# Kernel optimization log

Measured on AMD Instinct MI355X. Metric: run time of the kernel, lower is better.

## Reference

```python
import jax, jax.numpy as jnp
import numpy as np

B, N, C, K, KS, OC = 8, 4096, 64, 20, 16, 64


def setup_inputs() -> dict:
    key = jax.random.key(0)
    ks = jax.random.split(key, 6)
    return {
        'x': jax.random.normal(ks[0], (B, 3, N), jnp.float32),
        'feature': jax.random.normal(ks[1], (B, C, N), jnp.float32),
        'kernals': jax.random.normal(ks[2], (3, KS), jnp.float32),
        'mlp_w': jax.random.normal(ks[3], (C, 7), jnp.float32) * 0.1,
        'mlp_b': jnp.zeros((C,), jnp.float32),
        'conv_w': jax.random.normal(ks[4], (OC, 2 * C * KS), jnp.float32) * 0.02,
        'conv_b': jnp.zeros((OC,), jnp.float32),
        'bn_gamma': jnp.ones((OC,), jnp.float32),
        'bn_beta': jnp.zeros((OC,), jnp.float32),
    }


def reference(x, feature, kernals, mlp_w, mlp_b, conv_w, conv_b, bn_gamma, bn_beta):
    b, _, n = x.shape
    c = feature.shape[1]
    ksz = kernals.shape[1]
    k = K
    # ---- knn on coords ----
    xt = jnp.swapaxes(x, 1, 2)                      # [B,N,3]
    inner = -2.0 * jnp.einsum('bnc,bmc->bnm', xt, xt)
    xx = jnp.sum(xt * xt, axis=-1)                  # [B,N]
    pd = -xx[:, :, None] - inner - xx[:, None, :]   # negative squared dist
    idx = jax.lax.top_k(pd, k)[1]                   # [B,N,K] nearest (incl. self)
    gather = jax.vmap(lambda pts, i: pts[i])        # per-batch gather
    # ---- geometric features ----
    x_sp = gather(xt, idx)                          # [B,N,K,3]
    x_rel = x_sp - x_sp[:, :, 0:1, :]               # [B,N,K,3]
    x_dis = jnp.linalg.norm(x_rel, axis=-1, keepdims=True)
    center = jnp.broadcast_to(x_sp[:, :, 0:1, :], x_sp.shape)
    x_feats7 = jnp.concatenate([center, x_rel, x_dis], axis=-1)  # [B,N,K,7]
    # Conv1d(7,C,1) == pointwise linear over the 7 channels
    x_feats = jnp.einsum('bnkc,oc->bnok', x_feats7, mlp_w) + mlp_b[None, None, :, None]  # [B,N,C,K]
    # ---- neighbor feature gather ----
    ft = jnp.swapaxes(feature, 1, 2)                # [B,N,C]
    sp_f = gather(ft, idx)                          # [B,N,K,C]
    spirals = jnp.concatenate([jnp.swapaxes(sp_f, 2, 3), x_feats], axis=2)  # [B,N,2C,K]
    # ---- adjacency weights ----
    one_pad = jnp.zeros((k, ksz), jnp.float32).at[0, 0].set(1.0)
    aw = jnp.einsum('bnkc,cs->bnks', x_rel, kernals) + one_pad   # [B,N,K,KS]
    aw = jnp.where(aw > 0, aw, 0.0)
    aw = aw / (jnp.sum(aw, axis=2, keepdims=True) + 1e-6)
    aw = aw * aw
    aw = aw / (jnp.sum(aw, axis=2, keepdims=True) + 1e-6)
    aw = jnp.where(aw > 0.1, aw, 0.0)
    # ---- weighted aggregation + linear ----
    agg = jnp.einsum('bnck,bnks->bncs', spirals, aw)             # [B,N,2C,KS]
    agg = agg.reshape(b, n, 2 * c * ksz)
    out = agg @ conv_w.T + conv_b                                # [B,N,OC]
    out = jnp.swapaxes(out, 1, 2)                                # [B,OC,N]
    # ---- BatchNorm1d (training-mode batch statistics, eps=1e-5) ----
    mean = jnp.mean(out, axis=(0, 2), keepdims=True)
    var = jnp.var(out, axis=(0, 2), keepdims=True)
    out = (out - mean) / jnp.sqrt(var + 1e-5)
    out = out * bn_gamma[None, :, None] + bn_beta[None, :, None]
    return out
```

## Files before the change

kernel.cpp:

```cpp
#include <hip/hip_runtime.h>
#include <cfloat>
#include <math.h>

#define NB 8
#define NPT 4096
#define NC 64
#define KNN 20
#define KSZ 16
#define BPTS 8

typedef __attribute__((ext_vector_type(8))) short short8;
typedef __attribute__((ext_vector_type(4))) float f32x4;

__device__ __forceinline__ unsigned short f2bf(float f) {
  unsigned u = __float_as_uint(f);
  unsigned r = (u + 0x7fffu + ((u >> 16) & 1u)) >> 16;
  return (unsigned short)r;
}
__device__ __forceinline__ float bf2f(unsigned short h) {
  return __uint_as_float(((unsigned)h) << 16);
}

__global__ void k_pack_cw(const float* __restrict__ cw, unsigned short* __restrict__ bp) {
  int t = blockIdx.x * 256 + threadIdx.x;
  int j = t & 7, lane = (t >> 3) & 63, nt = (t >> 9) & 3, ks = t >> 11;
  int k = ks * 32 + ((lane >> 4) << 3) + j;
  int o = nt * 16 + (lane & 15);
  bp[t] = f2bf(cw[o * 2048 + k]);
}

__global__ void k_pack_cw2(const float* __restrict__ cw, const float* __restrict__ mlp_w,
                           const float* __restrict__ mlp_b, unsigned short* __restrict__ bp2) {
  int t = blockIdx.x * 256 + threadIdx.x;
  int jj = t & 7, lane = (t >> 3) & 63, nt = (t >> 9) & 3, ks2 = t >> 11;
  int k = ks2 * 32 + ((lane >> 4) << 3) + jj;
  int s = k >> 3, j = k & 7;
  int o = nt * 16 + (lane & 15);
  float acc = 0.0f;
  for (int c = 0; c < 64; ++c) {
    float coef = (j < 7) ? mlp_w[c * 7 + j] : mlp_b[c];
    acc = fmaf(cw[o * 2048 + 1024 + c * 16 + s], coef, acc);
  }
  bp2[t] = f2bf(acc);
}

__global__ void k_transpose_ft(const float* __restrict__ f, unsigned short* __restrict__ ft) {
  __shared__ float tile[64][65];
  int b = blockIdx.x >> 6;
  int n0 = (blockIdx.x & 63) * 64;
  int lane = threadIdx.x & 63;
  int rr = threadIdx.x >> 6;
#pragma unroll
  for (int c0 = 0; c0 < 64; c0 += 4) {
    int c = c0 + rr;
    tile[c][lane] = f[(b * 64 + c) * 4096 + n0 + lane];
  }
  __syncthreads();
#pragma unroll
  for (int m0 = 0; m0 < 64; m0 += 4) {
    int nn = m0 + rr;
    ft[(b * 4096 + n0 + nn) * 64 + lane] = f2bf(tile[lane][nn]);
  }
}

__device__ __noinline__ void knn_full(const float4* __restrict__ pts, int n, int lane,
                                      int g, int* __restrict__ idxOut) {
  const int M = 24;
  float4 qp = pts[n];
  float qx = qp.x, qy = qp.y, qz = qp.z;
  float v[M];
  int id[M];
#pragma unroll
  for (int r = 0; r < M; ++r) { v[r] = FLT_MAX; id[r] = 0x7fffffff; }
  for (int i = 0; i < 64; ++i) {
    int j = (i << 6) | lane;
    float4 p = pts[j];
    float dx = p.x - qx, dy = p.y - qy, dz = p.z - qz;
    float d2 = fmaf(dx, dx, fmaf(dy, dy, dz * dz));
    bool c[M];
#pragma unroll
    for (int r = 0; r < M; ++r) c[r] = d2 < v[r];
#pragma unroll
    for (int r = M - 1; r >= 1; --r) {
      v[r] = c[r - 1] ? v[r - 1] : (c[r] ? d2 : v[r]);
      id[r] = c[r - 1] ? id[r - 1] : (c[r] ? j : id[r]);
    }
    v[0] = c[0] ? d2 : v[0];
    id[0] = c[0] ? j : id[0];
  }
  unsigned long long key = ((unsigned long long)__float_as_uint(v[0]) << 32) | (unsigned)id[0];
  unsigned long long ext = ~0ull;
  for (int r = 0; r < 24; ++r) {
    unsigned long long k = key;
#pragma unroll
    for (int s = 1; s < 64; s <<= 1) {
      unsigned long long o = __shfl_xor(k, s, 64);
      k = (o < k) ? o : k;
    }
    if (lane == r) ext = k;
    if (key == k) {
#pragma unroll
      for (int q = 0; q < M - 1; ++q) { v[q] = v[q + 1]; id[q] = id[q + 1]; }
      v[M - 1] = FLT_MAX;
      id[M - 1] = 0x7fffffff;
      key = ((unsigned long long)__float_as_uint(v[0]) << 32) | (unsigned)id[0];
    }
  }
  int ei = (int)(unsigned)(ext & 0xffffffffu);
  bool al = lane < 24;
  double dv = -1.0;
  if (al) {
    float4 p = pts[ei];
    double dx = (double)p.x - (double)qx;
    double dy = (double)p.y - (double)qy;
    double dz = (double)p.z - (double)qz;
    dv = dx * dx + dy * dy + dz * dz;
  }
#pragma unroll
  for (int r = 0; r < 4; ++r) {
    double bd = al ? dv : -1.0;
    int bi = al ? ei : -1;
#pragma unroll
    for (int s = 1; s < 64; s <<= 1) {
      double od = __shfl_xor(bd, s, 64);
      int oi = __shfl_xor(bi, s, 64);
      if (od > bd || (od == bd && oi > bi)) { bd = od; bi = oi; }
    }
    if (al && ei == bi) al = false;
  }
  unsigned long long msk = __ballot(al && ei != n);
  if (al) {
    if (ei == n) {
      idxOut[g * 20] = n;
    } else {
      int pos = 1 + __popcll(msk & ((1ull << lane) - 1ull));
      idxOut[g * 20 + pos] = ei;
    }
  }
}

__launch_bounds__(1024, 8)
__global__ void k_knn(const float* __restrict__ x, int* __restrict__ idxOut) {
  __shared__ float4 pts[4096];
  int b = blockIdx.x >> 8;
  const float* xb = x + b * 3 * 4096;
  for (int i = threadIdx.x; i < 4096; i += 1024) {
    float px = xb[i], py = xb[4096 + i], pz = xb[8192 + i];
    pts[i] = make_float4(px, py, pz, fmaf(px, px, fmaf(py, py, pz * pz)));
  }
  __syncthreads();

  int lane = threadIdx.x & 63;
  int n = ((blockIdx.x & 255) << 4) + (threadIdx.x >> 6);
  int g = b * 4096 + n;

  float4 qp = pts[n];
  float m2x = -2.0f * qp.x, m2y = -2.0f * qp.y, m2z = -2.0f * qp.z;

  float v = FLT_MAX;
#pragma unroll 4
  for (int i = 0; i < 64; ++i) {
    float4 p = pts[(i << 6) | lane];
    float d = fmaf(m2z, p.z, fmaf(m2y, p.y, fmaf(m2x, p.x, p.w)));
    v = fminf(v, d);
  }

#pragma unroll
  for (int k = 2; k <= 64; k <<= 1) {
#pragma unroll
    for (int j = k >> 1; j > 0; j >>= 1) {
      float o = __shfl_xor(v, j, 64);
      bool up = ((lane & k) == 0);
      bool lower = ((lane & j) == 0);
      float mn = fminf(v, o), mx = fmaxf(v, o);
      v = (up == lower) ? mn : mx;
    }
  }
  float T = __shfl(v, 23, 64);

  int ei = -1;
  int base = 0;
  bool ovf = false;
#pragma unroll 2
  for (int i = 0; i < 64; ++i) {
    int j = (i << 6) | lane;
    float4 p = pts[j];
    float d = fmaf(m2z, p.z, fmaf(m2y, p.y, fmaf(m2x, p.x, p.w)));
    bool pred = (d <= T);
    unsigned long long mask = __ballot(pred);
    if (mask) {
      int cnt = __popcll(mask);
      if (base + cnt > 63) {
        ovf = true;
      } else {
        int dst = pred ? (base + __popcll(mask & ((1ull << lane) - 1ull))) : 63;
        int got = __builtin_amdgcn_ds_permute(dst << 2, j);
        bool recv = (lane >= base) && (lane < base + cnt);
        ei = recv ? got : ei;
      }
      base += cnt;
    }
  }

  bool ok = !ovf;
  if (ok) {
    bool act = lane < base;
    double dm = 1e300;
    if (act) {
      float4 p = pts[ei];
      double dx = (double)p.x - (double)qp.x;
      double dy = (double)p.y - (double)qp.y;
      double dz = (double)p.z - (double)qp.z;
      dm = dx * dx + dy * dy + dz * dz;
    }
    int rank = 0;
    for (int r = 0; r < base; ++r) {
      double dr = __shfl(dm, r, 64);
      int ir = __shfl(ei, r, 64);
      bool less = (dr < dm) || (dr == dm && ir < ei);
      rank += less ? 1 : 0;
    }
    bool keep = act && (rank < 20);
    bool isSelf = keep && (ei == n);
    unsigned long long smask = __ballot(isSelf);
    ok = (smask != 0ull);
    if (ok) {
      if (isSelf) idxOut[g * 20] = n;
      unsigned long long msk = __ballot(keep && !isSelf);
      if (keep && !isSelf) {
        int pos = 1 + __popcll(msk & ((1ull << lane) - 1ull));
        idxOut[g * 20 + pos] = ei;
      }
    }
  }
  if (!ok) knn_full(pts, n, lane, g, idxOut);
}

__launch_bounds__(256, 4)
__global__ void k_main(const float* __restrict__ x, const float* __restrict__ feat,
                       const unsigned short* __restrict__ ftT, int useFtT,
                       const float* __restrict__ kern,
                       const unsigned short* __restrict__ bpk,
                       const unsigned short* __restrict__ bpk2,
                       const float* __restrict__ conv_b, const int* __restrict__ idxIn,
                       float* __restrict__ out) {
  __shared__ __align__(16) unsigned short agg[BPTS][1024];
  __shared__ float awL[BPTS][20][16];
  __shared__ __align__(16) float4 f7s[BPTS][20];
  __shared__ __align__(16) unsigned short fpA[16][128];
  __shared__ __align__(16) float4 qL[BPTS];
  __shared__ int idxL[BPTS][20];

  int t = threadIdx.x;
  int lane = t & 63;
  int w = t >> 6;
  int b = blockIdx.x & 7;
  int n0 = (blockIdx.x >> 3) * BPTS;
  int g0 = b * 4096 + n0;
  const float* xb = x + b * 3 * 4096;

  {
    int pt = t >> 5, slot = t & 31;
    int n = n0 + pt;
    float qx = xb[n], qy = xb[4096 + n], qz = xb[8192 + n];
    if (slot < 20) {
      int kk = idxIn[(g0 + pt) * 20 + slot];
      idxL[pt][slot] = kk;
      float rx = xb[kk] - qx, ry = xb[4096 + kk] - qy, rz = xb[8192 + kk] - qz;
      float ds = sqrtf(rx * rx + ry * ry + rz * rz);
      f7s[pt][slot] = make_float4(rx, ry, rz, ds);
    } else if (slot == 20) {
      qL[pt] = make_float4(qx, qy, qz, 0.0f);
    }
  }
  __syncthreads();

  if (t < 128) {
    int pt = t >> 4, s = t & 15;
    float kx = kern[s], ky = kern[16 + s], kz = kern[32 + s];
    float wv[20];
#pragma unroll
    for (int k = 0; k < 20; ++k) {
      float4 f = f7s[pt][k];
      float dot = f.x * kx + f.y * ky + f.z * kz;
      if (s == 0 && k == 0) dot += 1.0f;
      wv[k] = dot > 0.0f ? dot : 0.0f;
    }
    float sum = 0.0f;
#pragma unroll
    for (int k = 0; k < 20; ++k) sum += wv[k];
    float inv1 = 1.0f / (sum + 1e-6f);
    float sum2 = 0.0f;
#pragma unroll
    for (int k = 0; k < 20; ++k) {
      float u = wv[k] * inv1;
      sum2 += u * u;
    }
    float inv2 = 1.0f / (sum2 + 1e-6f);
    float colsum = 0.0f;
    float F0 = 0.0f, F1 = 0.0f, F2 = 0.0f, F3 = 0.0f;
#pragma unroll
    for (int k = 0; k < 20; ++k) {
      float u = wv[k] * inv1;
      u = u * u * inv2;
      u = (u > 0.1f) ? u : 0.0f;
      awL[pt][k][s] = u;
      colsum += u;
      float4 f = f7s[pt][k];
      F0 = fmaf(f.x, u, F0);
      F1 = fmaf(f.y, u, F1);
      F2 = fmaf(f.z, u, F2);
      F3 = fmaf(f.w, u, F3);
    }
    float4 q = qL[pt];
    __align__(16) unsigned short tmp[8];
    tmp[0] = f2bf(q.x * colsum);
    tmp[1] = f2bf(q.y * colsum);
    tmp[2] = f2bf(q.z * colsum);
    tmp[3] = f2bf(F0);
    tmp[4] = f2bf(F1);
    tmp[5] = f2bf(F2);
    tmp[6] = f2bf(F3);
    tmp[7] = f2bf(colsum);
    *(uint4*)((char*)&fpA[0][0] + pt * 256 + ((s ^ (pt & 7)) << 4)) = *(uint4*)tmp;
  }
  __syncthreads();

#pragma unroll
  for (int half = 0; half < 2; ++half) {
    int pt = (w << 1) + half;
    int c = lane;
    float fv[20];
    if (useFtT) {
#pragma unroll
      for (int k = 0; k < 20; ++k) fv[k] = bf2f(ftT[(b * 4096 + idxL[pt][k]) * 64 + c]);
    } else {
      const float* fb = feat + (b * 64 + c) * 4096;
#pragma unroll
      for (int k = 0; k < 20; ++k) fv[k] = fb[idxL[pt][k]];
    }
    float a1[16];
#pragma unroll
    for (int s = 0; s < 16; ++s) a1[s] = 0.0f;
#pragma unroll
    for (int k = 0; k < 20; ++k) {
      float a = fv[k];
#pragma unroll
      for (int s = 0; s < 16; ++s) a1[s] = fmaf(a, awL[pt][k][s], a1[s]);
    }
    __align__(16) unsigned short tmp[16];
#pragma unroll
    for (int s = 0; s < 16; ++s) tmp[s] = f2bf(a1[s]);
    char* rb = (char*)&agg[pt][0];
    int sw = (pt & 7) << 4;
    *(uint4*)(rb + ((c * 32) ^ sw)) = *(uint4*)&tmp[0];
    *(uint4*)(rb + ((c * 32 + 16) ^ sw)) = *(uint4*)&tmp[8];
  }
  __syncthreads();

  f32x4 acc[4];
#pragma unroll
  for (int nt = 0; nt < 4; ++nt) acc[nt] = (f32x4){0.f, 0.f, 0.f, 0.f};
  {
    int r = lane & 15;
    const char* rowbase = (const char*)&agg[0][0] + r * 2048;
#pragma unroll
    for (int ks = 0; ks < 8; ++ks) {
      int ksl = w * 8 + ks;
      int off = (ksl * 64 + ((lane >> 4) << 4)) ^ ((r & 7) << 4);
      short8 af = *(const short8*)(rowbase + off);
#pragma unroll
      for (int nt = 0; nt < 4; ++nt) {
        short8 bf = *(const short8*)(bpk + (((ksl * 4 + nt) * 64 + lane) << 3));
        acc[nt] = __builtin_amdgcn_mfma_f32_16x16x32_bf16(af, bf, acc[nt], 0, 0, 0);
      }
    }
    {
      int chunk = (w << 2) + (lane >> 4);
      short8 af = *(const short8*)((const char*)&fpA[0][0] + r * 256 + ((chunk ^ (r & 7)) << 4));
#pragma unroll
      for (int nt = 0; nt < 4; ++nt) {
        short8 bf = *(const short8*)(bpk2 + ((((w << 2) + nt) * 64 + lane) << 3));
        acc[nt] = __builtin_amdgcn_mfma_f32_16x16x32_bf16(af, bf, acc[nt], 0, 0, 0);
      }
    }
  }
  __syncthreads();

  float* red = (float*)&agg[0][0];
  {
#pragma unroll
    for (int nt = 0; nt < 4; ++nt)
#pragma unroll
      for (int r = 0; r < 4; ++r) {
        int row = ((lane >> 4) << 2) + r;
        if (row < 8) {
          int o = nt * 16 + (lane & 15);
          red[(w * 8 + row) * 64 + (o ^ ((row & 7) << 2))] = acc[nt][r];
        }
      }
  }
  __syncthreads();
#pragma unroll
  for (int rep = 0; rep < 2; ++rep) {
    int u = rep * 256 + t;
    int pt = u & 7, o = u >> 3;
    float s = conv_b[o];
#pragma unroll
    for (int w2 = 0; w2 < 4; ++w2) s += red[(w2 * 8 + pt) * 64 + (o ^ ((pt & 7) << 2))];
    out[(b * 64 + o) * 4096 + n0 + pt] = s;
  }
}

__global__ void k_bnstats(const float* __restrict__ out, const float* __restrict__ gamma,
                          const float* __restrict__ beta, float* __restrict__ stats) {
  __shared__ double rs[256], rq[256];
  int o = blockIdx.x;
  double s = 0.0, q = 0.0;
  for (int b = 0; b < 8; ++b) {
    const float* p = out + (b * 64 + o) * 4096;
    for (int i = threadIdx.x; i < 4096; i += 256) {
      double v = (double)p[i];
      s += v;
      q += v * v;
    }
  }
  rs[threadIdx.x] = s;
  rq[threadIdx.x] = q;
  __syncthreads();
  for (int st = 128; st > 0; st >>= 1) {
    if ((int)threadIdx.x < st) {
      rs[threadIdx.x] += rs[threadIdx.x + st];
      rq[threadIdx.x] += rq[threadIdx.x + st];
    }
    __syncthreads();
  }
  if (threadIdx.x == 0) {
    double mean = rs[0] / 32768.0;
    double var = rq[0] / 32768.0 - mean * mean;
    double inv = 1.0 / sqrt(var + 1e-5);
    double sc = (double)gamma[o] * inv;
    stats[o * 2] = (float)sc;
    stats[o * 2 + 1] = (float)((double)beta[o] - mean * sc);
  }
}

__global__ void k_bnapply(float* __restrict__ out, const float* __restrict__ stats) {
  int i = blockIdx.x * 256 + threadIdx.x;
  int o = (i >> 12) & 63;
  out[i] = fmaf(out[i], stats[o * 2], stats[o * 2 + 1]);
}

extern "C" void kernel_launch(void* const* d_in, const int* in_sizes, int n_in,
                              void* d_out, int out_size, void* d_ws, size_t ws_size,
                              hipStream_t stream) {
  const float* x = (const float*)d_in[0];
  const float* feat = (const float*)d_in[1];
  const float* kern = (const float*)d_in[2];
  const float* mlp_w = (const float*)d_in[3];
  const float* mlp_b = (const float*)d_in[4];
  const float* conv_w = (const float*)d_in[5];
  const float* conv_b = (const float*)d_in[6];
  const float* gamma = (const float*)d_in[7];
  const float* beta = (const float*)d_in[8];
  float* out = (float*)d_out;
  char* ws = (char*)d_ws;

  int* idx = (int*)ws;
  float* stats = (float*)(ws + 2621440);
  unsigned short* bpk = (unsigned short*)(ws + 2625536);
  unsigned short* bpk2 = (unsigned short*)(ws + 2756608);
  unsigned short* ftT = (unsigned short*)(ws + 2772992);
  int useFtT = (ws_size >= (size_t)(2772992 + 4194304)) ? 1 : 0;

  k_pack_cw<<<256, 256, 0, stream>>>(conv_w, bpk);
  k_pack_cw2<<<32, 256, 0, stream>>>(conv_w, mlp_w, mlp_b, bpk2);
  if (useFtT) k_transpose_ft<<<512, 256, 0, stream>>>(feat, ftT);
  k_knn<<<2048, 1024, 0, stream>>>(x, idx);
  k_main<<<4096, 256, 0, stream>>>(x, feat, ftT, useFtT, kern, bpk, bpk2,
                                   conv_b, idx, out);
  k_bnstats<<<64, 256, 0, stream>>>(out, gamma, beta, stats);
  k_bnapply<<<8192, 256, 0, stream>>>(out, stats);
}
```

Baseline: 210.5 us.

## Process four query points per wavefront in KNN to reuse candidate loads

```diff
diff --git a/kernel.cpp b/kernel.cpp
--- a/kernel.cpp
+++ b/kernel.cpp
@@ -139,10 +139,10 @@
   }
 }
 
-__launch_bounds__(1024, 8)
+__launch_bounds__(1024, 2)
 __global__ void k_knn(const float* __restrict__ x, int* __restrict__ idxOut) {
   __shared__ float4 pts[4096];
-  int b = blockIdx.x >> 8;
+  int b = blockIdx.x >> 6;
   const float* xb = x + b * 3 * 4096;
   for (int i = threadIdx.x; i < 4096; i += 1024) {
     float px = xb[i], py = xb[4096 + i], pz = xb[8192 + i];
@@ -151,89 +151,114 @@
   __syncthreads();
 
   int lane = threadIdx.x & 63;
-  int n = ((blockIdx.x & 255) << 4) + (threadIdx.x >> 6);
-  int g = b * 4096 + n;
-
-  float4 qp = pts[n];
-  float m2x = -2.0f * qp.x, m2y = -2.0f * qp.y, m2z = -2.0f * qp.z;
-
-  float v = FLT_MAX;
-#pragma unroll 4
+  int w = threadIdx.x >> 6;
+  int nb = ((blockIdx.x & 63) << 6) + (w << 2);
+  int gb = b * 4096 + nb;
+
+  float m2x[4], m2y[4], m2z[4];
+#pragma unroll
+  for (int r = 0; r < 4; ++r) {
+    float4 q = pts[nb + r];
+    m2x[r] = -2.0f * q.x;
+    m2y[r] = -2.0f * q.y;
+    m2z[r] = -2.0f * q.z;
+  }
+
+  float v[4];
+#pragma unroll
+  for (int r = 0; r < 4; ++r) v[r] = FLT_MAX;
+#pragma unroll 2
   for (int i = 0; i < 64; ++i) {
     float4 p = pts[(i << 6) | lane];
-    float d = fmaf(m2z, p.z, fmaf(m2y, p.y, fmaf(m2x, p.x, p.w)));
-    v = fminf(v, d);
+#pragma unroll
+    for (int r = 0; r < 4; ++r) {
+      float d = fmaf(m2z[r], p.z, fmaf(m2y[r], p.y, fmaf(m2x[r], p.x, p.w)));
+      v[r] = fminf(v[r], d);
+    }
   }
 
 #pragma unroll
   for (int k = 2; k <= 64; k <<= 1) {
 #pragma unroll
     for (int j = k >> 1; j > 0; j >>= 1) {
-      float o = __shfl_xor(v, j, 64);
-      bool up = ((lane & k) == 0);
-      bool lower = ((lane & j) == 0);
-      float mn = fminf(v, o), mx = fmaxf(v, o);
-      v = (up == lower) ? mn : mx;
-    }
-  }
-  float T = __shfl(v, 23, 64);
-
-  int ei = -1;
-  int base = 0;
-  bool ovf = false;
+      bool sel = ((lane & k) == 0) == ((lane & j) == 0);
+#pragma unroll
+      for (int r = 0; r < 4; ++r) {
+        float o = __shfl_xor(v[r], j, 64);
+        float mn = fminf(v[r], o), mx = fmaxf(v[r], o);
+        v[r] = sel ? mn : mx;
+      }
+    }
+  }
+  float T[4];
+#pragma unroll
+  for (int r = 0; r < 4; ++r) T[r] = __shfl(v[r], 23, 64);
+
+  int ei[4], base[4];
+  bool ovf[4];
+#pragma unroll
+  for (int r = 0; r < 4; ++r) { ei[r] = -1; base[r] = 0; ovf[r] = false; }
 #pragma unroll 2
   for (int i = 0; i < 64; ++i) {
-    int j = (i << 6) | lane;
-    float4 p = pts[j];
-    float d = fmaf(m2z, p.z, fmaf(m2y, p.y, fmaf(m2x, p.x, p.w)));
-    bool pred = (d <= T);
-    unsigned long long mask = __ballot(pred);
-    if (mask) {
-      int cnt = __popcll(mask);
-      if (base + cnt > 63) {
-        ovf = true;
-      } else {
-        int dst = pred ? (base + __popcll(mask & ((1ull << lane) - 1ull))) : 63;
-        int got = __builtin_amdgcn_ds_permute(dst << 2, j);
-        bool recv = (lane >= base) && (lane < base + cnt);
-        ei = recv ? got : ei;
-      }
-      base += cnt;
-    }
-  }
-
-  bool ok = !ovf;
-  if (ok) {
-    bool act = lane < base;
-    double dm = 1e300;
-    if (act) {
-      float4 p = pts[ei];
-      double dx = (double)p.x - (double)qp.x;
-      double dy = (double)p.y - (double)qp.y;
-      double dz = (double)p.z - (double)qp.z;
-      dm = dx * dx + dy * dy + dz * dz;
-    }
-    int rank = 0;
-    for (int r = 0; r < base; ++r) {
-      double dr = __shfl(dm, r, 64);
-      int ir = __shfl(ei, r, 64);
-      bool less = (dr < dm) || (dr == dm && ir < ei);
-      rank += less ? 1 : 0;
-    }
-    bool keep = act && (rank < 20);
-    bool isSelf = keep && (ei == n);
-    unsigned long long smask = __ballot(isSelf);
-    ok = (smask != 0ull);
+    float4 p = pts[(i << 6) | lane];
+#pragma unroll
+    for (int r = 0; r < 4; ++r) {
+      float d = fmaf(m2z[r], p.z, fmaf(m2y[r], p.y, fmaf(m2x[r], p.x, p.w)));
+      bool pred = (d <= T[r]);
+      unsigned long long mask = __ballot(pred);
+      if (mask) {
+        int cnt = __popcll(mask);
+        if (base[r] + cnt > 63) {
+          ovf[r] = true;
+        } else {
+          int dst = pred ? (base[r] + __popcll(mask & ((1ull << lane) - 1ull))) : 63;
+          int got = __builtin_amdgcn_ds_permute(dst << 2, (i << 6) | lane);
+          bool recv = (lane >= base[r]) && (lane < base[r] + cnt);
+          ei[r] = recv ? got : ei[r];
+        }
+        base[r] += cnt;
+      }
+    }
+  }
+
+#pragma unroll
+  for (int r = 0; r < 4; ++r) {
+    int n = nb + r, g = gb + r;
+    bool ok = !ovf[r];
     if (ok) {
-      if (isSelf) idxOut[g * 20] = n;
-      unsigned long long msk = __ballot(keep && !isSelf);
-      if (keep && !isSelf) {
-        int pos = 1 + __popcll(msk & ((1ull << lane) - 1ull));
-        idxOut[g * 20 + pos] = ei;
-      }
-    }
-  }
-  if (!ok) knn_full(pts, n, lane, g, idxOut);
+      float4 qp = pts[n];
+      bool act = lane < base[r];
+      int e = ei[r];
+      double dm = 1e300;
+      if (act) {
+        float4 p = pts[e];
+        double dx = (double)p.x - (double)qp.x;
+        double dy = (double)p.y - (double)qp.y;
+        double dz = (double)p.z - (double)qp.z;
+        dm = dx * dx + dy * dy + dz * dz;
+      }
+      int rank = 0;
+      for (int r2 = 0; r2 < base[r]; ++r2) {
+        double dr = __shfl(dm, r2, 64);
+        int ir = __shfl(e, r2, 64);
+        bool less = (dr < dm) || (dr == dm && ir < e);
+        rank += less ? 1 : 0;
+      }
+      bool keep = act && (rank < 20);
+      bool isSelf = keep && (e == n);
+      unsigned long long smask = __ballot(isSelf);
+      ok = (smask != 0ull);
+      if (ok) {
+        if (isSelf) idxOut[g * 20] = n;
+        unsigned long long msk = __ballot(keep && !isSelf);
+        if (keep && !isSelf) {
+          int pos = 1 + __popcll(msk & ((1ull << lane) - 1ull));
+          idxOut[g * 20 + pos] = e;
+        }
+      }
+    }
+    if (!ok) knn_full(pts, n, lane, g, idxOut);
+  }
 }
 
 __launch_bounds__(256, 4)
@@ -476,7 +501,7 @@
   k_pack_cw<<<256, 256, 0, stream>>>(conv_w, bpk);
   k_pack_cw2<<<32, 256, 0, stream>>>(conv_w, mlp_w, mlp_b, bpk2);
   if (useFtT) k_transpose_ft<<<512, 256, 0, stream>>>(feat, ftT);
-  k_knn<<<2048, 1024, 0, stream>>>(x, idx);
+  k_knn<<<512, 1024, 0, stream>>>(x, idx);
   k_main<<<4096, 256, 0, stream>>>(x, feat, ftT, useFtT, kern, bpk, bpk2,
                                    conv_b, idx, out);
   k_bnstats<<<64, 256, 0, stream>>>(out, gamma, beta, stats);
```

Result: faster. 202.1 us (-4.0%).
